# Kernel tuning notes

Measured on AMD Instinct MI355X. Metric: run time of the kernel, lower is better.

The kernel has to match this reference:

```python
import jax, jax.numpy as jnp
import numpy as np

OUT = 7      # roi_align output_size
RATIO = 2    # fixed sampling_ratio (torchvision default -1 is adaptive; fixed 2 used for jit-ability)
IMG = 518    # image size (DINOv2 patch 14 -> 37x37 feature grid)


def setup_inputs() -> dict:
    key = jax.random.key(0)
    ks = jax.random.split(key, 12)
    B, N, C, H, W = 4, 512, 256, 37, 37
    NUM_CLASSES = 91
    f0 = jax.random.normal(ks[0], (B, C, H, W), jnp.float32)
    f1 = jax.random.normal(ks[1], (B, C, H, W), jnp.float32)
    f2 = jax.random.normal(ks[2], (B, C, H, W), jnp.float32)
    f3 = jax.random.normal(ks[3], (B, C, H, W), jnp.float32)
    # proposals in image coords so areas span all 4 level buckets (32^2..128^2+)
    cx = jax.random.uniform(ks[4], (B, N)) * IMG
    cy = jax.random.uniform(ks[5], (B, N)) * IMG
    bw = jax.random.uniform(ks[6], (B, N)) * 248.0 + 8.0
    bh = jax.random.uniform(ks[7], (B, N)) * 248.0 + 8.0
    x1 = jnp.maximum(cx - 0.5 * bw, 0.0)
    y1 = jnp.maximum(cy - 0.5 * bh, 0.0)
    x2 = jnp.minimum(cx + 0.5 * bw, float(IMG))
    y2 = jnp.minimum(cy + 0.5 * bh, float(IMG))
    proposals = jnp.stack([x1, y1, x2, y2], axis=-1)  # [B,N,4]
    D = C * OUT * OUT  # 12544
    w1 = jax.random.normal(ks[8], (D, 1024), jnp.float32) * 0.02
    b1 = jnp.zeros((1024,), jnp.float32)
    w2 = jax.random.normal(ks[9], (1024, 1024), jnp.float32) * 0.02
    b2 = jnp.zeros((1024,), jnp.float32)
    wc = jax.random.normal(ks[10], (1024, NUM_CLASSES), jnp.float32) * 0.02
    bc = jnp.zeros((NUM_CLASSES,), jnp.float32)
    wb = jax.random.normal(ks[11], (1024, 4), jnp.float32) * 0.02
    bb = jnp.zeros((4,), jnp.float32)
    return {"f0": f0, "f1": f1, "f2": f2, "f3": f3, "proposals": proposals,
            "w1": w1, "b1": b1, "w2": w2, "b2": b2,
            "wc": wc, "bc": bc, "wb": wb, "bb": bb}


def _multilevel_roi_align(f0, f1, f2, f3, proposals):
    B, C, H, W = f0.shape
    N = proposals.shape[1]
    P = OUT * RATIO * OUT * RATIO
    # levels stacked along spatial axis: [B, C, 4*H*W]
    feats_cat = jnp.stack([f0, f1, f2, f3], axis=2).reshape(B, C, 4 * H * W)
    bw = proposals[..., 2] - proposals[..., 0]
    bh = proposals[..., 3] - proposals[..., 1]
    area = bw * bh
    # area-based FPN level: <32^2->0, <64^2->1, <128^2->2, else 3
    lvl = ((area >= 32.0 ** 2).astype(jnp.int32)
           + (area >= 64.0 ** 2).astype(jnp.int32)
           + (area >= 128.0 ** 2).astype(jnp.int32))  # [B,N]
    # roi_align, spatial_scale=1.0, aligned=True
    x1 = proposals[..., 0] - 0.5
    y1 = proposals[..., 1] - 0.5
    bin_w = bw / OUT
    bin_h = bh / OUT
    offs = jnp.arange(OUT, dtype=jnp.float32)[:, None] + (jnp.arange(RATIO, dtype=jnp.float32) + 0.5)[None, :] / RATIO  # [7,2]
    ys = y1[..., None, None] + offs * bin_h[..., None, None]  # [B,N,7,2]
    xs = x1[..., None, None] + offs * bin_w[..., None, None]  # [B,N,7,2]
    y = ys[..., :, :, None, None]  # [B,N,7,2,1,1]
    x = xs[..., None, None, :, :]  # [B,N,1,1,7,2]
    valid = ((y >= -1.0) & (y <= H) & (x >= -1.0) & (x <= W)).astype(f0.dtype)
    yc = jnp.clip(y, 0.0, H - 1.0)
    xc = jnp.clip(x, 0.0, W - 1.0)
    y0f = jnp.floor(yc)
    x0f = jnp.floor(xc)
    y0 = y0f.astype(jnp.int32)
    x0 = x0f.astype(jnp.int32)
    y1i = jnp.minimum(y0 + 1, H - 1)
    x1i = jnp.minimum(x0 + 1, W - 1)
    ly = yc - y0f
    lx = xc - x0f
    hy = 1.0 - ly
    hx = 1.0 - lx
    base = (lvl * (H * W))[:, :, None, None, None, None]
    shp = (B, N, OUT, RATIO, OUT, RATIO)

    def gather(yi, xi):
        idx = jnp.broadcast_to(base + yi * W + xi, shp).reshape(B, N * P)
        return jax.vmap(lambda fb, ib: jnp.take(fb, ib, axis=1))(feats_cat, idx)  # [B,C,N*P]

    def wflat(w):
        return jnp.broadcast_to(w * valid, shp).reshape(B, 1, N * P)

    acc = (wflat(hy * hx) * gather(y0, x0)
           + wflat(hy * lx) * gather(y0, x1i)
           + wflat(ly * hx) * gather(y1i, x0)
           + wflat(ly * lx) * gather(y1i, x1i))
    roi = acc.reshape(B, C, N, OUT, RATIO, OUT, RATIO).sum(axis=(4, 6)) / (RATIO * RATIO)
    return roi.transpose(0, 2, 1, 3, 4)  # [B,N,C,7,7]


def reference(f0, f1, f2, f3, proposals, w1, b1, w2, b2, wc, bc, wb, bb):
    B, N = proposals.shape[0], proposals.shape[1]
    roi = _multilevel_roi_align(f0, f1, f2, f3, proposals)  # [B,N,C,7,7]
    flat = roi.reshape(B * N, -1)  # torch flatten order matches [C,7,7]
    h1 = jax.nn.relu(flat @ w1 + b1)
    h2 = jax.nn.relu(h1 @ w2 + b2)
    scores = (h2 @ wc + bc).reshape(B, N, -1)
    bbox_deltas = (h2 @ wb + bb).reshape(B, N, 4)
    return scores, bbox_deltas
```

## Files before the change

kernel.cpp:

```cpp
#include <hip/hip_runtime.h>
#include <hip/hip_bf16.h>
#include <stdint.h>

#define FH 37
#define FW 37
#define FC 256
#define NB 4
#define NP 512
#define BNT (NB*NP)
#define KDIM (FC*49)
#define HID 1024
#define NHEAD 95
#define CAP 256

typedef __bf16 bf16x8 __attribute__((ext_vector_type(8)));
typedef float  f32x4  __attribute__((ext_vector_type(4)));

__global__ __launch_bounds__(256) void k_transpose(const float* __restrict__ f0,
                                                   const float* __restrict__ f1,
                                                   const float* __restrict__ f2,
                                                   const float* __restrict__ f3,
                                                   float* __restrict__ ft) {
  __shared__ float tile[32][33];
  int bl = blockIdx.z;
  int b = bl >> 2, l = bl & 3;
  const float* src = (l == 0 ? f0 : l == 1 ? f1 : l == 2 ? f2 : f3) + (size_t)b * FC * FH * FW;
  int yx0 = blockIdx.x * 32;
  int c0  = blockIdx.y * 32;
  int tx = threadIdx.x;
  int ty = threadIdx.y;
  #pragma unroll
  for (int i = 0; i < 32; i += 8) {
    int c  = c0 + ty + i;
    int yx = yx0 + tx;
    float v = (yx < FH * FW) ? src[(size_t)c * (FH * FW) + yx] : 0.f;
    tile[ty + i][tx] = v;
  }
  __syncthreads();
  #pragma unroll
  for (int i = 0; i < 32; i += 8) {
    int yx = yx0 + ty + i;
    int c  = c0 + tx;
    if (yx < FH * FW)
      ft[((size_t)bl * (FH * FW) + yx) * FC + c] = tile[tx][ty + i];
  }
}

__global__ __launch_bounds__(256) void k_compact(const float* __restrict__ props,
                                                 int* __restrict__ count,
                                                 int* __restrict__ list) {
  int bn = blockIdx.x * 256 + threadIdx.x;
  float px1 = props[(size_t)bn * 4 + 0];
  float py1 = props[(size_t)bn * 4 + 1];
  float px2 = props[(size_t)bn * 4 + 2];
  float py2 = props[(size_t)bn * 4 + 3];
  float bw = px2 - px1, bh = py2 - py1;
  float X1 = px1 - 0.5f, Y1 = py1 - 0.5f;
  float binw = bw * (1.f / 7.f), binh = bh * (1.f / 7.f);
  float sy0 = Y1 + ((float)0 * 0.5f + 0.25f) * binh;
  float sx0 = X1 + ((float)0 * 0.5f + 0.25f) * binw;
  bool active = (sy0 <= 37.f) && (sx0 <= 37.f);
  if (active) {
    int s = atomicAdd(count, 1);
    if (s < CAP) list[s] = bn;
  }
}

__global__ __launch_bounds__(256) void k_roi(const float* __restrict__ ft,
                                             const float* __restrict__ props,
                                             const int* __restrict__ count,
                                             const int* __restrict__ list,
                                             __hip_bfloat16* __restrict__ Ahi,
                                             __hip_bfloat16* __restrict__ Alo) {
  int s = blockIdx.x;
  int cnt = min(*count, CAP);
  if (s >= cnt) return;
  int bn = list[s];
  int b = bn >> 9;
  int p = blockIdx.y;
  int oy = p / 7, ox = p % 7;
  int c = threadIdx.x;

  float px1 = props[(size_t)bn * 4 + 0];
  float py1 = props[(size_t)bn * 4 + 1];
  float px2 = props[(size_t)bn * 4 + 2];
  float py2 = props[(size_t)bn * 4 + 3];
  float bw = px2 - px1, bh = py2 - py1;
  float area = bw * bh;
  int lvl = (area >= 1024.f) + (area >= 4096.f) + (area >= 16384.f);
  float X1 = px1 - 0.5f, Y1 = py1 - 0.5f;
  float binw = bw * (1.f / 7.f), binh = bh * (1.f / 7.f);
  int fbase = ((b * 4 + lvl) * (FH * FW)) * FC;

  float acc = 0.f;
  #pragma unroll
  for (int ry = 0; ry < 2; ++ry) {
    int iy = oy * 2 + ry;
    float sy = Y1 + ((float)iy * 0.5f + 0.25f) * binh;
    #pragma unroll
    for (int rx = 0; rx < 2; ++rx) {
      int ix = ox * 2 + rx;
      float sx = X1 + ((float)ix * 0.5f + 0.25f) * binw;
      float valid = (sy >= -1.f && sy <= 37.f && sx >= -1.f && sx <= 37.f) ? 0.25f : 0.f;
      float yc = fminf(fmaxf(sy, 0.f), 36.f);
      float xc = fminf(fmaxf(sx, 0.f), 36.f);
      float y0f = floorf(yc), x0f = floorf(xc);
      int y0 = (int)y0f, x0 = (int)x0f;
      int y1i = min(y0 + 1, 36), x1i = min(x0 + 1, 36);
      float ly = yc - y0f, lx = xc - x0f;
      float hy = 1.f - ly, hx = 1.f - lx;
      float w00 = hy * hx * valid, w01 = hy * lx * valid;
      float w10 = ly * hx * valid, w11 = ly * lx * valid;
      if (w00 != 0.f) acc += w00 * ft[fbase + (y0  * FW + x0 ) * FC + c];
      if (w01 != 0.f) acc += w01 * ft[fbase + (y0  * FW + x1i) * FC + c];
      if (w10 != 0.f) acc += w10 * ft[fbase + (y1i * FW + x0 ) * FC + c];
      if (w11 != 0.f) acc += w11 * ft[fbase + (y1i * FW + x1i) * FC + c];
    }
  }
  size_t o = (size_t)s * KDIM + (size_t)c * 49 + p;
  __hip_bfloat16 h = __float2bfloat16(acc);
  Ahi[o] = h;
  Alo[o] = __float2bfloat16(acc - __bfloat162float(h));
}

__global__ __launch_bounds__(256, 2) void k_gemm_fused(
    const __hip_bfloat16* __restrict__ Ahi,
    const __hip_bfloat16* __restrict__ Alo,
    const float* __restrict__ Wf,
    float* __restrict__ part,
    const int* __restrict__ countPtr,
    int Kt, int kChunk) {
  int cnt = min(*countPtr, CAP);
  if ((int)blockIdx.x * 128 >= cnt) return;
  __shared__ __align__(16) char lds[65536];
  const int t = threadIdx.x, lane = t & 63, wave = t >> 6;
  const int m0 = blockIdx.x * 128, n0 = blockIdx.y * 128;
  const int kStart = blockIdx.z * kChunk;
  const int niters = kChunk >> 5;

  const int nn = t & 127;
  const int kq = t >> 7;

  const int wm = (wave >> 1) * 64, wn = (wave & 1) * 64;
  const int rsel = lane & 15, q = lane >> 4;

  f32x4 acc[4][4];
  #pragma unroll
  for (int m = 0; m < 4; ++m)
    #pragma unroll
    for (int n = 0; n < 4; ++n)
      acc[m][n] = (f32x4){0.f, 0.f, 0.f, 0.f};

  auto loadB = [&](float* v, int k0) {
    const float* p = Wf + (size_t)(k0 + kq * 16) * HID + n0 + nn;
    #pragma unroll
    for (int j = 0; j < 16; ++j) v[j] = p[(size_t)j * HID];
  };

  auto writeB = [&](int buf, const float* v) {
    char* bh = lds + buf * 32768 + 16384;
    char* bl = lds + buf * 32768 + 24576;
    #pragma unroll
    for (int hh = 0; hh < 2; ++hh) {
      bf16x8 hv, lv;
      #pragma unroll
      for (int e = 0; e < 8; ++e) {
        float f = v[hh * 8 + e];
        __hip_bfloat16 h = __float2bfloat16(f);
        float fr = f - __bfloat162float(h);
        __hip_bfloat16 l2 = __float2bfloat16(fr);
        hv[e] = *reinterpret_cast<__bf16*>(&h);
        lv[e] = *reinterpret_cast<__bf16*>(&l2);
      }
      int oct = kq * 2 + hh;
      int off = nn * 64 + ((oct ^ (nn & 3)) << 4);
      *(bf16x8*)(bh + off) = hv;
      *(bf16x8*)(bl + off) = lv;
    }
  };

  auto stageA = [&](int buf, int k0) {
    #pragma unroll
    for (int pl = 0; pl < 2; ++pl) {
      const __hip_bfloat16* src = pl ? Alo : Ahi;
      #pragma unroll
      for (int i = 0; i < 2; ++i) {
        int seg = wave * 2 + i;
        int row = seg * 16 + (lane >> 2);
        int cq = (lane & 3) ^ (row & 3);
        const char* g = (const char*)(src + (size_t)(m0 + row) * Kt + k0 + cq * 8);
        char* l = lds + buf * 32768 + pl * 8192 + seg * 1024;
        __builtin_amdgcn_global_load_lds((const unsigned int __attribute__((address_space(1)))*)g,
                                         (unsigned int __attribute__((address_space(3)))*)l,
                                         16, 0, 0);
      }
    }
  };

  auto compute = [&](int buf) {
    const char* base = lds + buf * 32768;
    bf16x8 ah[4], al2[4], bh2[4], bl2[4];
    #pragma unroll
    for (int mf = 0; mf < 4; ++mf) {
      int row = wm + mf * 16 + rsel;
      int off = row * 64 + ((q ^ (row & 3)) << 4);
      ah[mf]  = *(const bf16x8*)(base + off);
      al2[mf] = *(const bf16x8*)(base + 8192 + off);
    }
    #pragma unroll
    for (int nf = 0; nf < 4; ++nf) {
      int col = wn + nf * 16 + rsel;
      int off = col * 64 + ((q ^ (col & 3)) << 4);
      bh2[nf] = *(const bf16x8*)(base + 16384 + off);
      bl2[nf] = *(const bf16x8*)(base + 24576 + off);
    }
    #pragma unroll
    for (int mf = 0; mf < 4; ++mf)
      #pragma unroll
      for (int nf = 0; nf < 4; ++nf) {
        acc[mf][nf] = __builtin_amdgcn_mfma_f32_16x16x32_bf16(ah[mf],  bh2[nf], acc[mf][nf], 0, 0, 0);
        acc[mf][nf] = __builtin_amdgcn_mfma_f32_16x16x32_bf16(ah[mf],  bl2[nf], acc[mf][nf], 0, 0, 0);
        acc[mf][nf] = __builtin_amdgcn_mfma_f32_16x16x32_bf16(al2[mf], bh2[nf], acc[mf][nf], 0, 0, 0);
      }
  };

  float vA[16], vB[16];
  loadB(vA, kStart);
  stageA(0, kStart);
  writeB(0, vA);
  __syncthreads();

  int k = kStart;
  const int npair = niters >> 1;
  for (int pr = 0; pr < npair; ++pr) {
    loadB(vB, k + 32);
    stageA(1, k + 32);
    compute(0);
    writeB(1, vB);
    __syncthreads();
    bool more = (pr + 1 < npair);
    if (more) {
      loadB(vA, k + 64);
      stageA(0, k + 64);
    }
    compute(1);
    if (more) writeB(0, vA);
    __syncthreads();
    k += 64;
  }

  float* pbase = part + (size_t)blockIdx.z * (CAP * HID);
  #pragma unroll
  for (int mf = 0; mf < 4; ++mf)
    #pragma unroll
    for (int nf = 0; nf < 4; ++nf) {
      int row = m0 + wm + mf * 16 + q * 4;
      int col = n0 + wn + nf * 16 + rsel;
      #pragma unroll
      for (int r = 0; r < 4; ++r)
        pbase[(size_t)(row + r) * HID + col] = acc[mf][nf][r];
    }
}

__global__ __launch_bounds__(256) void k_reduce1(const float* __restrict__ part,
                                                 const float* __restrict__ bias,
                                                 const int* __restrict__ countPtr,
                                                 int S,
                                                 __hip_bfloat16* __restrict__ Hhi,
                                                 __hip_bfloat16* __restrict__ Hlo) {
  int cnt = min(*countPtr, CAP);
  if ((int)(blockIdx.x >> 2) >= cnt) return;
  size_t i = (size_t)blockIdx.x * 256 + threadIdx.x;
  const size_t tot = (size_t)CAP * HID;
  int col = (int)(i & (HID - 1));
  float a = bias[col];
  for (int s = 0; s < S; ++s) a += part[(size_t)s * tot + i];
  a = fmaxf(a, 0.f);
  __hip_bfloat16 h = __float2bfloat16(a);
  Hhi[i] = h;
  Hlo[i] = __float2bfloat16(a - __bfloat162float(h));
}

__global__ __launch_bounds__(256) void k_h2c(const float* __restrict__ w2,
                                             const float* __restrict__ b1,
                                             float* __restrict__ h2cr) {
  int n = blockIdx.x * 256 + threadIdx.x;
  int k0 = blockIdx.y * 128;
  float acc = 0.f;
  for (int k = k0; k < k0 + 128; ++k)
    acc += fmaxf(b1[k], 0.f) * w2[(size_t)k * HID + n];
  atomicAdd(&h2cr[n], acc);
}

__global__ __launch_bounds__(256) void k_outc(const float* __restrict__ h2cr,
                                              const float* __restrict__ b2,
                                              const float* __restrict__ wc,
                                              const float* __restrict__ bc,
                                              const float* __restrict__ wb,
                                              const float* __restrict__ bb,
                                              float* __restrict__ outc) {
  __shared__ float red[4];
  int j = blockIdx.x;
  int t = threadIdx.x;
  float acc = 0.f;
  for (int n = t; n < HID; n += 256) {
    float h = fmaxf(b2[n] + h2cr[n], 0.f);
    float w = (j < 91) ? wc[(size_t)n * 91 + j] : wb[(size_t)n * 4 + (j - 91)];
    acc += h * w;
  }
  #pragma unroll
  for (int o = 32; o; o >>= 1) acc += __shfl_down(acc, o, 64);
  if ((t & 63) == 0) red[t >> 6] = acc;
  __syncthreads();
  if (t == 0) {
    float bj = (j < 91) ? bc[j] : bb[j - 91];
    outc[j] = bj + red[0] + red[1] + red[2] + red[3];
  }
}

__global__ __launch_bounds__(256) void k_fill(const float* __restrict__ outc,
                                              float* __restrict__ out) {
  int i = blockIdx.x * 256 + threadIdx.x;
  const int SC = BNT * 91;
  if (i < SC) out[i] = outc[i % 91];
  else {
    int r = i - SC;
    if (r < BNT * 4) out[SC + r] = outc[91 + (r & 3)];
  }
}

__global__ __launch_bounds__(256) void k_head(const float* __restrict__ part,
                                              const float* __restrict__ b2,
                                              const float* __restrict__ wc,
                                              const float* __restrict__ bc,
                                              const float* __restrict__ wb,
                                              const float* __restrict__ bb,
                                              const int* __restrict__ count,
                                              const int* __restrict__ list,
                                              float* __restrict__ out) {
  __shared__ float row[HID];
  int s = blockIdx.x;
  int cnt = min(*count, CAP);
  if (s >= cnt) return;
  int bn = list[s];
  int t = threadIdx.x;
  const size_t tot = (size_t)CAP * HID;
  #pragma unroll
  for (int j = 0; j < 4; ++j) {
    int col = t + j * 256;
    float a = b2[col];
    #pragma unroll
    for (int ss = 0; ss < 8; ++ss) a += part[(size_t)ss * tot + (size_t)s * HID + col];
    row[col] = fmaxf(a, 0.f);
  }
  __syncthreads();
  if (t < NHEAD) {
    float acc = (t < 91) ? bc[t] : bb[t - 91];
    if (t < 91) {
      for (int k = 0; k < HID; ++k) acc += row[k] * wc[(size_t)k * 91 + t];
      out[(size_t)bn * 91 + t] = acc;
    } else {
      for (int k = 0; k < HID; ++k) acc += row[k] * wb[(size_t)k * 4 + (t - 91)];
      out[(size_t)BNT * 91 + (size_t)bn * 4 + (t - 91)] = acc;
    }
  }
}

extern "C" void kernel_launch(void* const* d_in, const int* in_sizes, int n_in,
                              void* d_out, int out_size, void* d_ws, size_t ws_size,
                              hipStream_t stream) {
  const float* f0    = (const float*)d_in[0];
  const float* f1    = (const float*)d_in[1];
  const float* f2    = (const float*)d_in[2];
  const float* f3    = (const float*)d_in[3];
  const float* props = (const float*)d_in[4];
  const float* w1    = (const float*)d_in[5];
  const float* b1    = (const float*)d_in[6];
  const float* w2    = (const float*)d_in[7];
  const float* b2    = (const float*)d_in[8];
  const float* wc    = (const float*)d_in[9];
  const float* bc    = (const float*)d_in[10];
  const float* wb    = (const float*)d_in[11];
  const float* bb    = (const float*)d_in[12];
  float* out = (float*)d_out;

  char* ws = (char*)d_ws;
  size_t off = 0;
  auto alloc = [&](size_t bytes) -> char* {
    char* p = ws + off;
    off += (bytes + 255) & ~(size_t)255;
    return p;
  };
  float*          ft    = (float*)         alloc((size_t)16 * FH * FW * FC * 4);
  __hip_bfloat16* Ahi   = (__hip_bfloat16*)alloc((size_t)CAP * KDIM * 2);
  __hip_bfloat16* Alo   = (__hip_bfloat16*)alloc((size_t)CAP * KDIM * 2);
  float*          part  = (float*)         alloc((size_t)28 * CAP * HID * 4);
  __hip_bfloat16* H1hi  = (__hip_bfloat16*)alloc((size_t)CAP * HID * 2);
  __hip_bfloat16* H1lo  = (__hip_bfloat16*)alloc((size_t)CAP * HID * 2);
  float*          h2cr  = (float*)         alloc(HID * 4);
  int*            count = (int*)           alloc(256);
  int*            list  = (int*)           alloc(CAP * 4);
  float*          outc  = (float*)         alloc(NHEAD * 4);
  (void)ws_size; (void)in_sizes; (void)n_in; (void)out_size;

  hipMemsetAsync(h2cr, 0, HID * 4 + 256, stream);

  k_transpose<<<dim3(43, 8, 16), dim3(32, 8), 0, stream>>>(f0, f1, f2, f3, ft);
  k_compact<<<8, 256, 0, stream>>>(props, count, list);
  k_roi<<<dim3(CAP, 49), 256, 0, stream>>>(ft, props, count, list, Ahi, Alo);

  k_h2c<<<dim3(4, 8), 256, 0, stream>>>(w2, b1, h2cr);
  k_outc<<<NHEAD, 256, 0, stream>>>(h2cr, b2, wc, bc, wb, bb, outc);
  k_fill<<<760, 256, 0, stream>>>(outc, out);

  k_gemm_fused<<<dim3(CAP / 128, 8, 28), 256, 0, stream>>>(Ahi, Alo, w1, part, count,
                                                           KDIM, 448);
  k_reduce1<<<CAP * HID / 256, 256, 0, stream>>>(part, b1, count, 28, H1hi, H1lo);
  k_gemm_fused<<<dim3(CAP / 128, 8, 8), 256, 0, stream>>>(H1hi, H1lo, w2, part, count,
                                                          HID, 128);
  k_head<<<CAP, 256, 0, stream>>>(part, b2, wc, bc, wb, bb, count, list, out);
}
```

Before: 237.1 us.

## Shrink GEMM tile to 64x64 with k=64 single buffer, widen h2c grid

The split-bf16 GEMM drops from 128x128 tiles with a double-buffered k=32 pipeline to 64x64 tiles with a single-buffered k=64 stage. This roughly halves LDS use, raises the occupancy hint to 4 blocks per SIMD, and launches four times as many blocks, so the GEMM can cover more CUs when only a few rows are valid. The cost is lost load/compute overlap, lower per-block data reuse, and more total W1 traffic. Separately, k_h2c is split over 64 k-chunks instead of 8 to get more parallelism, at the price of more atomic adds.

```diff
diff --git a/kernel.cpp b/kernel.cpp
--- a/kernel.cpp
+++ b/kernel.cpp
@@ -123,7 +123,7 @@
   Alo[o] = __float2bfloat16(acc - __bfloat162float(h));
 }
 
-__global__ __launch_bounds__(256, 2) void k_gemm_fused(
+__global__ __launch_bounds__(256, 4) void k_gemm_fused(
     const __hip_bfloat16* __restrict__ Ahi,
     const __hip_bfloat16* __restrict__ Alo,
     const float* __restrict__ Wf,
@@ -131,129 +131,104 @@
     const int* __restrict__ countPtr,
     int Kt, int kChunk) {
   int cnt = min(*countPtr, CAP);
-  if ((int)blockIdx.x * 128 >= cnt) return;
-  __shared__ __align__(16) char lds[65536];
+  const int m0 = blockIdx.x * 64;
+  if (m0 >= cnt) return;
+  __shared__ __align__(16) char lds[32768];
   const int t = threadIdx.x, lane = t & 63, wave = t >> 6;
-  const int m0 = blockIdx.x * 128, n0 = blockIdx.y * 128;
+  const int n0 = blockIdx.y * 64;
   const int kStart = blockIdx.z * kChunk;
-  const int niters = kChunk >> 5;
-
-  const int nn = t & 127;
-  const int kq = t >> 7;
-
-  const int wm = (wave >> 1) * 64, wn = (wave & 1) * 64;
+  const int niters = kChunk >> 6;
+
+  const int nc = lane;
+  const int wq = wave;
+
+  const int wm = (wave & 1) * 32, wn = (wave >> 1) * 32;
   const int rsel = lane & 15, q = lane >> 4;
 
-  f32x4 acc[4][4];
-  #pragma unroll
-  for (int m = 0; m < 4; ++m)
-    #pragma unroll
-    for (int n = 0; n < 4; ++n)
+  f32x4 acc[2][2];
+  #pragma unroll
+  for (int m = 0; m < 2; ++m)
+    #pragma unroll
+    for (int n = 0; n < 2; ++n)
       acc[m][n] = (f32x4){0.f, 0.f, 0.f, 0.f};
 
-  auto loadB = [&](float* v, int k0) {
-    const float* p = Wf + (size_t)(k0 + kq * 16) * HID + n0 + nn;
-    #pragma unroll
-    for (int j = 0; j < 16; ++j) v[j] = p[(size_t)j * HID];
-  };
-
-  auto writeB = [&](int buf, const float* v) {
-    char* bh = lds + buf * 32768 + 16384;
-    char* bl = lds + buf * 32768 + 24576;
-    #pragma unroll
-    for (int hh = 0; hh < 2; ++hh) {
-      bf16x8 hv, lv;
-      #pragma unroll
-      for (int e = 0; e < 8; ++e) {
-        float f = v[hh * 8 + e];
-        __hip_bfloat16 h = __float2bfloat16(f);
-        float fr = f - __bfloat162float(h);
-        __hip_bfloat16 l2 = __float2bfloat16(fr);
-        hv[e] = *reinterpret_cast<__bf16*>(&h);
-        lv[e] = *reinterpret_cast<__bf16*>(&l2);
-      }
-      int oct = kq * 2 + hh;
-      int off = nn * 64 + ((oct ^ (nn & 3)) << 4);
-      *(bf16x8*)(bh + off) = hv;
-      *(bf16x8*)(bl + off) = lv;
-    }
-  };
-
-  auto stageA = [&](int buf, int k0) {
+  for (int it = 0; it < niters; ++it) {
+    int k0 = kStart + it * 64;
     #pragma unroll
     for (int pl = 0; pl < 2; ++pl) {
       const __hip_bfloat16* src = pl ? Alo : Ahi;
       #pragma unroll
       for (int i = 0; i < 2; ++i) {
         int seg = wave * 2 + i;
-        int row = seg * 16 + (lane >> 2);
-        int cq = (lane & 3) ^ (row & 3);
-        const char* g = (const char*)(src + (size_t)(m0 + row) * Kt + k0 + cq * 8);
-        char* l = lds + buf * 32768 + pl * 8192 + seg * 1024;
+        int row = seg * 8 + (lane >> 3);
+        int j   = lane & 7;
+        int gch = (j & 4) | ((j & 3) ^ (row & 3));
+        const char* g = (const char*)(src + (size_t)(m0 + row) * Kt + k0 + gch * 8);
+        char* l = lds + pl * 8192 + seg * 1024;
         __builtin_amdgcn_global_load_lds((const unsigned int __attribute__((address_space(1)))*)g,
                                          (unsigned int __attribute__((address_space(3)))*)l,
                                          16, 0, 0);
       }
     }
-  };
-
-  auto compute = [&](int buf) {
-    const char* base = lds + buf * 32768;
-    bf16x8 ah[4], al2[4], bh2[4], bl2[4];
-    #pragma unroll
-    for (int mf = 0; mf < 4; ++mf) {
-      int row = wm + mf * 16 + rsel;
-      int off = row * 64 + ((q ^ (row & 3)) << 4);
-      ah[mf]  = *(const bf16x8*)(base + off);
-      al2[mf] = *(const bf16x8*)(base + 8192 + off);
-    }
-    #pragma unroll
-    for (int nf = 0; nf < 4; ++nf) {
-      int col = wn + nf * 16 + rsel;
-      int off = col * 64 + ((q ^ (col & 3)) << 4);
-      bh2[nf] = *(const bf16x8*)(base + 16384 + off);
-      bl2[nf] = *(const bf16x8*)(base + 24576 + off);
-    }
-    #pragma unroll
-    for (int mf = 0; mf < 4; ++mf)
-      #pragma unroll
-      for (int nf = 0; nf < 4; ++nf) {
-        acc[mf][nf] = __builtin_amdgcn_mfma_f32_16x16x32_bf16(ah[mf],  bh2[nf], acc[mf][nf], 0, 0, 0);
-        acc[mf][nf] = __builtin_amdgcn_mfma_f32_16x16x32_bf16(ah[mf],  bl2[nf], acc[mf][nf], 0, 0, 0);
-        acc[mf][nf] = __builtin_amdgcn_mfma_f32_16x16x32_bf16(al2[mf], bh2[nf], acc[mf][nf], 0, 0, 0);
+    {
+      float v[16];
+      const float* p = Wf + (size_t)(k0 + wq * 16) * HID + n0 + nc;
+      #pragma unroll
+      for (int j = 0; j < 16; ++j) v[j] = p[(size_t)j * HID];
+      #pragma unroll
+      for (int jj = 0; jj < 2; ++jj) {
+        bf16x8 hv, lv;
+        #pragma unroll
+        for (int e = 0; e < 8; ++e) {
+          float f = v[jj * 8 + e];
+          __hip_bfloat16 h = __float2bfloat16(f);
+          float fr = f - __bfloat162float(h);
+          __hip_bfloat16 l2 = __float2bfloat16(fr);
+          hv[e] = *reinterpret_cast<__bf16*>(&h);
+          lv[e] = *reinterpret_cast<__bf16*>(&l2);
+        }
+        int c  = wq * 2 + jj;
+        int cs = (c & 4) | ((c & 3) ^ (nc & 3));
+        int off = nc * 128 + cs * 16;
+        *(bf16x8*)(lds + 16384 + off) = hv;
+        *(bf16x8*)(lds + 24576 + off) = lv;
       }
-  };
-
-  float vA[16], vB[16];
-  loadB(vA, kStart);
-  stageA(0, kStart);
-  writeB(0, vA);
-  __syncthreads();
-
-  int k = kStart;
-  const int npair = niters >> 1;
-  for (int pr = 0; pr < npair; ++pr) {
-    loadB(vB, k + 32);
-    stageA(1, k + 32);
-    compute(0);
-    writeB(1, vB);
+    }
     __syncthreads();
-    bool more = (pr + 1 < npair);
-    if (more) {
-      loadB(vA, k + 64);
-      stageA(0, k + 64);
-    }
-    compute(1);
-    if (more) writeB(0, vA);
+    #pragma unroll
+    for (int kk = 0; kk < 2; ++kk) {
+      bf16x8 ah[2], al2[2], bh2[2], bl2[2];
+      #pragma unroll
+      for (int mf = 0; mf < 2; ++mf) {
+        int row = wm + mf * 16 + rsel;
+        int off = row * 128 + ((kk * 4 + (q ^ (row & 3))) << 4);
+        ah[mf]  = *(const bf16x8*)(lds + off);
+        al2[mf] = *(const bf16x8*)(lds + 8192 + off);
+      }
+      #pragma unroll
+      for (int nf = 0; nf < 2; ++nf) {
+        int col = wn + nf * 16 + rsel;
+        int off = col * 128 + ((kk * 4 + (q ^ (col & 3))) << 4);
+        bh2[nf] = *(const bf16x8*)(lds + 16384 + off);
+        bl2[nf] = *(const bf16x8*)(lds + 24576 + off);
+      }
+      #pragma unroll
+      for (int mf = 0; mf < 2; ++mf)
+        #pragma unroll
+        for (int nf = 0; nf < 2; ++nf) {
+          acc[mf][nf] = __builtin_amdgcn_mfma_f32_16x16x32_bf16(ah[mf],  bh2[nf], acc[mf][nf], 0, 0, 0);
+          acc[mf][nf] = __builtin_amdgcn_mfma_f32_16x16x32_bf16(ah[mf],  bl2[nf], acc[mf][nf], 0, 0, 0);
+          acc[mf][nf] = __builtin_amdgcn_mfma_f32_16x16x32_bf16(al2[mf], bh2[nf], acc[mf][nf], 0, 0, 0);
+        }
+    }
     __syncthreads();
-    k += 64;
   }
 
   float* pbase = part + (size_t)blockIdx.z * (CAP * HID);
   #pragma unroll
-  for (int mf = 0; mf < 4; ++mf)
-    #pragma unroll
-    for (int nf = 0; nf < 4; ++nf) {
+  for (int mf = 0; mf < 2; ++mf)
+    #pragma unroll
+    for (int nf = 0; nf < 2; ++nf) {
       int row = m0 + wm + mf * 16 + q * 4;
       int col = n0 + wn + nf * 16 + rsel;
       #pragma unroll
@@ -285,9 +260,10 @@
                                              const float* __restrict__ b1,
                                              float* __restrict__ h2cr) {
   int n = blockIdx.x * 256 + threadIdx.x;
-  int k0 = blockIdx.y * 128;
+  int k0 = blockIdx.y * 16;
   float acc = 0.f;
-  for (int k = k0; k < k0 + 128; ++k)
+  #pragma unroll
+  for (int k = k0; k < k0 + 16; ++k)
     acc += fmaxf(b1[k], 0.f) * w2[(size_t)k * HID + n];
   atomicAdd(&h2cr[n], acc);
 }
@@ -409,14 +385,14 @@
   k_compact<<<8, 256, 0, stream>>>(props, count, list);
   k_roi<<<dim3(CAP, 49), 256, 0, stream>>>(ft, props, count, list, Ahi, Alo);
 
-  k_h2c<<<dim3(4, 8), 256, 0, stream>>>(w2, b1, h2cr);
+  k_h2c<<<dim3(4, 64), 256, 0, stream>>>(w2, b1, h2cr);
   k_outc<<<NHEAD, 256, 0, stream>>>(h2cr, b2, wc, bc, wb, bb, outc);
   k_fill<<<760, 256, 0, stream>>>(outc, out);
 
-  k_gemm_fused<<<dim3(CAP / 128, 8, 28), 256, 0, stream>>>(Ahi, Alo, w1, part, count,
+  k_gemm_fused<<<dim3(CAP / 64, 16, 28), 256, 0, stream>>>(Ahi, Alo, w1, part, count,
                                                            KDIM, 448);
   k_reduce1<<<CAP * HID / 256, 256, 0, stream>>>(part, b1, count, 28, H1hi, H1lo);
-  k_gemm_fused<<<dim3(CAP / 128, 8, 8), 256, 0, stream>>>(H1hi, H1lo, w2, part, count,
+  k_gemm_fused<<<dim3(CAP / 64, 16, 8), 256, 0, stream>>>(H1hi, H1lo, w2, part, count,
                                                           HID, 128);
   k_head<<<CAP, 256, 0, stream>>>(part, b2, wc, bc, wb, bb, count, list, out);
 }
```

Measured after the change: 239.2 us. About the same (+0.9%).
